# Kernel optimization log

Hardware: AMD Instinct MI355X
Metric: run time of the kernel (lower is better)

The kernel has to match this reference:

```python
import jax, jax.numpy as jnp
import numpy as np

EPS = 1e-6

def rms_norm(x, scale):
    # qwen3_compatible: compute in fp32 (inputs already fp32)
    ms = jnp.mean(x * x, axis=-1, keepdims=True)
    return x * jax.lax.rsqrt(ms + EPS) * scale

def apply_rope(x, cos, sin):
    # x: [b, h, s, hd]; cos/sin: [s, hd]
    hd = x.shape[-1]
    x1, x2 = x[..., : hd // 2], x[..., hd // 2 :]
    rotated = jnp.concatenate([-x2, x1], axis=-1)
    return x * cos[None, None] + rotated * sin[None, None]

def setup_inputs() -> dict:
    key = jax.random.key(0)
    ks = jax.random.split(key, 8)
    b, s, d_in, nh, kv, hd = 2, 2048, 2048, 16, 4, 128
    d_out = nh * hd
    x = jax.random.normal(ks[0], (b, s, d_in), jnp.float32)
    # causal mask: True = masked (future positions)
    mask = jnp.triu(jnp.ones((s, s), bool), k=1)
    # RoPE tables (standard rotary frequencies)
    inv_freq = 1.0 / (10000.0 ** (np.arange(0, hd, 2, dtype=np.float32) / hd))
    angles = np.arange(s, dtype=np.float32)[:, None] * inv_freq[None, :]  # [s, hd/2]
    angles = np.concatenate([angles, angles], axis=1)  # [s, hd]
    cos = jnp.asarray(np.cos(angles))
    sin = jnp.asarray(np.sin(angles))
    sc = 0.02
    Wq = jax.random.normal(ks[1], (d_in, d_out), jnp.float32) * sc
    Wk = jax.random.normal(ks[2], (d_in, kv * hd), jnp.float32) * sc
    Wv = jax.random.normal(ks[3], (d_in, kv * hd), jnp.float32) * sc
    Wo = jax.random.normal(ks[4], (d_out, d_in), jnp.float32) * sc
    q_scale = jnp.ones((hd,), jnp.float32)
    k_scale = jnp.ones((hd,), jnp.float32)
    return {"x": x, "mask": mask, "cos": cos, "sin": sin, "Wq": Wq, "Wk": Wk,
            "Wv": Wv, "Wo": Wo, "q_scale": q_scale, "k_scale": k_scale}

def reference(x, mask, cos, sin, Wq, Wk, Wv, Wo, q_scale, k_scale):
    b, s, d_in = x.shape
    nh, kv, hd = 16, 4, 128
    g = nh // kv  # group_size
    # projections (Linear, no bias); weights stored as [in, out]
    q = (x @ Wq).reshape(b, s, nh, hd).transpose(0, 2, 1, 3)   # [b, nh, s, hd]
    k = (x @ Wk).reshape(b, s, kv, hd).transpose(0, 2, 1, 3)   # [b, kv, s, hd]
    v = (x @ Wv).reshape(b, s, kv, hd).transpose(0, 2, 1, 3)   # [b, kv, s, hd]
    q = rms_norm(q, q_scale)
    k = rms_norm(k, k_scale)
    q = apply_rope(q, cos, sin)
    k = apply_rope(k, cos, sin)
    # group queries: head h uses kv group h // g (repeat_interleave semantics)
    qg = q.reshape(b, kv, g, s, hd)
    scores = jnp.einsum('bkgqh,bkth->bkgqt', qg, k) / jnp.sqrt(jnp.float32(hd))
    scores = jnp.where(mask[None, None, None], -jnp.inf, scores)
    w = jax.nn.softmax(scores, axis=-1)
    ctx = jnp.einsum('bkgqt,bkth->bkgqh', w, v)                # [b, kv, g, s, hd]
    ctx = ctx.reshape(b, nh, s, hd).transpose(0, 2, 1, 3).reshape(b, s, nh * hd)
    return ctx @ Wo
```

## Files before the change

### kernel.cpp

```cpp
#include <hip/hip_runtime.h>
#include <hip/hip_bf16.h>
#include <math.h>

#define B  2
#define S  2048
#define D  2048
#define NH 16
#define KV 4
#define HD 128
#define G  (NH / KV)
#define M_ROWS (B * S)

typedef __hip_bfloat16 bf16;
typedef __attribute__((ext_vector_type(8))) short s16x8;
typedef __attribute__((ext_vector_type(4))) float f32x4;

__device__ __forceinline__ short bf16_bits(float f) {
    bf16 t = __float2bfloat16(f);
    return *reinterpret_cast<short*>(&t);
}

__device__ __forceinline__ void gload16(const void* g, void* l) {
    __builtin_amdgcn_global_load_lds(
        (const __attribute__((address_space(1))) void*)g,
        (__attribute__((address_space(3))) void*)l, 16, 0, 0);
}

__global__ __launch_bounds__(256) void cast_f32_bf16(const float* __restrict__ in,
                                                     bf16* __restrict__ o, int n4) {
    int i = blockIdx.x * 256 + threadIdx.x;
    if (i >= n4) return;
    float4 v = ((const float4*)in)[i];
    ushort4 u;
    u.x = (unsigned short)bf16_bits(v.x);
    u.y = (unsigned short)bf16_bits(v.y);
    u.z = (unsigned short)bf16_bits(v.z);
    u.w = (unsigned short)bf16_bits(v.w);
    ((ushort4*)o)[i] = u;
}

__global__ __launch_bounds__(256) void tcast(const float* __restrict__ W,
                                             bf16* __restrict__ Wt, int K, int N) {
    __shared__ float T[32][33];
    const int n0 = blockIdx.x * 32, k0 = blockIdx.y * 32;
    const int tx = threadIdx.x & 31, ty = threadIdx.x >> 5;
#pragma unroll
    for (int i = 0; i < 4; i++)
        T[ty + i * 8][tx] = W[(size_t)(k0 + ty + i * 8) * N + n0 + tx];
    __syncthreads();
#pragma unroll
    for (int i = 0; i < 4; i++)
        Wt[(size_t)(n0 + ty + i * 8) * K + k0 + tx] = __float2bfloat16(T[tx][ty + i * 8]);
}

template<int MODE>
__global__ __launch_bounds__(256) void gemm_bt(const bf16* __restrict__ A,
                                               const bf16* __restrict__ Bt,
                                               void* __restrict__ out0,
                                               void* __restrict__ out1,
                                               void* __restrict__ out2,
                                               int N, int K) {
    const int m0 = blockIdx.y * 128;
    const int n0 = blockIdx.x * 128;
    const int tid  = threadIdx.x;
    const int wave = tid >> 6;
    const int lane = tid & 63;
    const int mw = (wave >> 1) * 64;
    const int nw = (wave & 1) * 64;

    __shared__ short Al[128 * 32];
    __shared__ short Bl[128 * 32];

    f32x4 acc[4][4] = {};

    const int fr = lane & 15;
    const int fq = (lane >> 4) * 8;

    const int r0  = wave * 32;
    const int srl = lane >> 2;
    const int scl = (lane & 3) * 8;

    for (int k0 = 0; k0 < K; k0 += 32) {
        __syncthreads();
        gload16(A  + (size_t)(m0 + r0 +      srl) * K + k0 + scl, &Al[(r0     ) * 32]);
        gload16(A  + (size_t)(m0 + r0 + 16 + srl) * K + k0 + scl, &Al[(r0 + 16) * 32]);
        gload16(Bt + (size_t)(n0 + r0 +      srl) * K + k0 + scl, &Bl[(r0     ) * 32]);
        gload16(Bt + (size_t)(n0 + r0 + 16 + srl) * K + k0 + scl, &Bl[(r0 + 16) * 32]);
        __syncthreads();

        s16x8 af[4], bfr[4];
#pragma unroll
        for (int i = 0; i < 4; i++) {
            af[i]  = *(const s16x8*)(&Al[(mw + i * 16 + fr) * 32 + fq]);
            bfr[i] = *(const s16x8*)(&Bl[(nw + i * 16 + fr) * 32 + fq]);
        }
#pragma unroll
        for (int i = 0; i < 4; i++)
#pragma unroll
            for (int j = 0; j < 4; j++)
                acc[i][j] = __builtin_amdgcn_mfma_f32_16x16x32_bf16(af[i], bfr[j], acc[i][j], 0, 0, 0);
    }

    const int col_l = lane & 15;
    const int row_l = (lane >> 4) * 4;
#pragma unroll
    for (int i = 0; i < 4; i++)
#pragma unroll
        for (int j = 0; j < 4; j++) {
            int m_base = m0 + mw + i * 16 + row_l;
            int n = n0 + nw + j * 16 + col_l;
            if (MODE == 3 && n >= 2560) {
                int nn = n - 2560;
                int bb = m_base >> 11, si = m_base & (S - 1);
                int hh = nn >> 7, d = nn & (HD - 1);
                ushort4 u;
                u.x = (unsigned short)bf16_bits(acc[i][j][0]);
                u.y = (unsigned short)bf16_bits(acc[i][j][1]);
                u.z = (unsigned short)bf16_bits(acc[i][j][2]);
                u.w = (unsigned short)bf16_bits(acc[i][j][3]);
                *(ushort4*)((bf16*)out2 + (((size_t)(bb * KV + hh)) * HD + d) * S + si) = u;
            } else {
#pragma unroll
                for (int r = 0; r < 4; r++) {
                    int m = m_base + r;
                    if (MODE == 3) {
                        int bb = m >> 11, si = m & (S - 1);
                        if (n < 2048) {
                            int h = n >> 7, d = n & (HD - 1);
                            ((float*)out0)[(((size_t)(bb * NH + h)) * S + si) * HD + d] = acc[i][j][r];
                        } else {
                            int nn = n - 2048;
                            int h = nn >> 7, d = nn & (HD - 1);
                            ((float*)out1)[(((size_t)(bb * KV + h)) * S + si) * HD + d] = acc[i][j][r];
                        }
                    } else {
                        ((float*)out0)[(size_t)m * N + n] = acc[i][j][r];
                    }
                }
            }
        }
}

template<bool SC>
__global__ __launch_bounds__(256) void rms_rope2(const float* __restrict__ in,
                                                 bf16* __restrict__ out,
                                                 const float* __restrict__ scale,
                                                 const float* __restrict__ cosT,
                                                 const float* __restrict__ sinT) {
    const int row  = blockIdx.x * 4 + (threadIdx.x >> 6);
    const int lane = threadIdx.x & 63;
    const int si   = row & (S - 1);
    const float* rp = in + (size_t)row * HD;

    float x1 = rp[lane];
    float x2 = rp[lane + 64];

    float ss = x1 * x1 + x2 * x2;
#pragma unroll
    for (int m = 1; m < 64; m <<= 1) ss += __shfl_xor(ss, m, 64);
    const float rinv = rsqrtf(ss * (1.0f / HD) + 1e-6f);

    const float n1 = x1 * rinv * scale[lane];
    const float n2 = x2 * rinv * scale[lane + 64];

    const float c = cosT[(size_t)si * HD + lane];
    const float s = sinT[(size_t)si * HD + lane];

    float r1 = n1 * c - n2 * s;
    float r2 = n2 * c + n1 * s;
    if (SC) { r1 *= 0.08838834764831845f; r2 *= 0.08838834764831845f; }

    out[(size_t)row * HD + lane]      = __float2bfloat16(r1);
    out[(size_t)row * HD + lane + 64] = __float2bfloat16(r2);
}

__global__ __launch_bounds__(512) void flash_mfma4(const bf16* __restrict__ qb,
                                                   const bf16* __restrict__ kb,
                                                   const bf16* __restrict__ vtb,
                                                   bf16* __restrict__ ctx) {
    const int p    = blockIdx.x;
    const int kvh  = blockIdx.y;
    const int b    = blockIdx.z;
    const int tid  = threadIdx.x;
    const int wave = tid >> 6;
    const int grp  = wave >> 2;
    const int wl   = wave & 3;
    const int lane = tid & 63;
    const int tg   = tid & 255;
    const int quad = lane >> 4;
    const int l16  = lane & 15;
    const int quad8 = quad * 8;
    const int h = kvh * G + wl;

    __shared__ __align__(16) char pool[108544];
    short* KsG = (short*)(pool + grp * 17408);
    short* VsG = (short*)(pool + 34816 + grp * 18432);
    short* PsW = (short*)(pool + 71680 + wave * 4608);
    float* oS  = (float*)pool;
    float* lS  = (float*)(pool + 65536);

    const bf16* qbase = qb  + ((size_t)(b * NH + h))   * S * HD;
    const bf16* kbase = kb  + ((size_t)(b * KV + kvh)) * S * HD;
    const bf16* vbase = vtb + ((size_t)(b * KV + kvh)) * HD * S;

    const int nA   = (p >> 1) + 1;
    const int pB   = 63 - p;
    const int iBeg = grp ? 17 : 0;
    const int iEnd = grp ? 33 : 17;

    int q0 = grp ? 32 * pB : 32 * p;

    s16x8 qf[2][4];
#pragma unroll
    for (int s = 0; s < 2; s++) {
        const bf16* qrow = qbase + (size_t)(q0 + s * 16 + l16) * HD + quad8;
#pragma unroll
        for (int ks = 0; ks < 4; ks++)
            qf[s][ks] = *(const s16x8*)(qrow + ks * 32);
    }

    f32x4 o[2][8] = {};
    float l[2][4] = {};

    uint4 kreg[4], vreg[4];
    {
        const int tf = (iBeg < nA) ? 64 * iBeg : 64 * (iBeg - nA);
#pragma unroll
        for (int it = 0; it < 4; it++) {
            int c = tg + it * 256;
            kreg[it] = *(const uint4*)(kbase + (size_t)(tf + (c >> 4)) * HD + (c & 15) * 8);
            vreg[it] = *(const uint4*)(vbase + (size_t)(c >> 3) * S + tf + (c & 7) * 8);
        }
    }

    for (int ii = 0; ii < 17; ii++) {
        const int i   = iBeg + ii;
        const bool act = (i < iEnd);

        if (act) {
#pragma unroll
            for (int it = 0; it < 4; it++) {
                int c = tg + it * 256;
                *(uint4*)&KsG[(c >> 4) * 136 + (c & 15) * 8] = kreg[it];
                *(uint4*)&VsG[(c >> 3) * 72  + (c & 7)  * 8] = vreg[it];
            }
        }
        __syncthreads();

        const int t0 = (i < nA) ? 64 * i : 64 * (i - nA);

        if (act && i + 1 < iEnd) {
            const int tn = (i + 1 < nA) ? 64 * (i + 1) : 64 * (i + 1 - nA);
#pragma unroll
            for (int it = 0; it < 4; it++) {
                int c = tg + it * 256;
                kreg[it] = *(const uint4*)(kbase + (size_t)(tn + (c >> 4)) * HD + (c & 15) * 8);
                vreg[it] = *(const uint4*)(vbase + (size_t)(c >> 3) * S + tn + (c & 7) * 8);
            }
        }

        if (act) {
            f32x4 sa[2][4] = {};
#pragma unroll
            for (int ks = 0; ks < 4; ks++) {
#pragma unroll
                for (int n = 0; n < 4; n++) {
                    s16x8 kf = *(const s16x8*)&KsG[(n * 16 + l16) * 136 + ks * 32 + quad8];
#pragma unroll
                    for (int s = 0; s < 2; s++)
                        sa[s][n] = __builtin_amdgcn_mfma_f32_16x16x32_bf16(qf[s][ks], kf, sa[s][n], 0, 0, 0);
                }
            }

            const bool msk = (t0 + 63 > q0);
#pragma unroll
            for (int s = 0; s < 2; s++)
#pragma unroll
                for (int r = 0; r < 4; r++) {
                    const int qg = q0 + s * 16 + quad * 4 + r;
#pragma unroll
                    for (int n = 0; n < 4; n++) {
                        float v = sa[s][n][r];
                        if (msk && (t0 + n * 16 + l16 > qg)) v = -INFINITY;
                        float pv = __expf(v - 13.0f);
                        l[s][r] += pv;
                        PsW[(s * 16 + quad * 4 + r) * 72 + n * 16 + l16] = bf16_bits(pv);
                    }
                }

#pragma unroll
            for (int ks = 0; ks < 2; ks++) {
                s16x8 vf[8];
#pragma unroll
                for (int n = 0; n < 8; n++)
                    vf[n] = *(const s16x8*)&VsG[(n * 16 + l16) * 72 + ks * 32 + quad8];
#pragma unroll
                for (int s = 0; s < 2; s++) {
                    s16x8 pf = *(const s16x8*)&PsW[(s * 16 + l16) * 72 + ks * 32 + quad8];
#pragma unroll
                    for (int n = 0; n < 8; n++)
                        o[s][n] = __builtin_amdgcn_mfma_f32_16x16x32_bf16(pf, vf[n], o[s][n], 0, 0, 0);
                }
            }

            if (i == nA - 1) {
#pragma unroll
                for (int s = 0; s < 2; s++)
#pragma unroll
                    for (int r = 0; r < 4; r++) {
                        float ls = l[s][r];
#pragma unroll
                        for (int m = 1; m < 16; m <<= 1) ls += __shfl_xor(ls, m, 64);
                        const float inv = 1.0f / ls;
                        const int qg = q0 + s * 16 + quad * 4 + r;
                        bf16* dst = ctx + (((size_t)(b * S + qg)) * NH + h) * HD;
#pragma unroll
                        for (int n = 0; n < 8; n++)
                            dst[n * 16 + l16] = __float2bfloat16(o[s][n][r] * inv);
                    }
                q0 = 32 * pB;
#pragma unroll
                for (int s = 0; s < 2; s++) {
                    const bf16* qrow = qbase + (size_t)(q0 + s * 16 + l16) * HD + quad8;
#pragma unroll
                    for (int ks = 0; ks < 4; ks++)
                        qf[s][ks] = *(const s16x8*)(qrow + ks * 32);
                }
#pragma unroll
                for (int s = 0; s < 2; s++) {
#pragma unroll
                    for (int n = 0; n < 8; n++) o[s][n] = (f32x4){0.f, 0.f, 0.f, 0.f};
#pragma unroll
                    for (int r = 0; r < 4; r++) l[s][r] = 0.0f;
                }
            }
        }

        __syncthreads();
    }

    if (grp == 1) {
        float* oW = oS + wl * 64 * 64;
        float* lW = lS + wl * 8 * 64;
#pragma unroll
        for (int s = 0; s < 2; s++)
#pragma unroll
            for (int n = 0; n < 8; n++)
#pragma unroll
                for (int r = 0; r < 4; r++)
                    oW[((s * 8 + n) * 4 + r) * 64 + lane] = o[s][n][r];
#pragma unroll
        for (int s = 0; s < 2; s++)
#pragma unroll
            for (int r = 0; r < 4; r++)
                lW[(s * 4 + r) * 64 + lane] = l[s][r];
    }
    __syncthreads();
    if (grp == 0) {
        float* oW = oS + wl * 64 * 64;
        float* lW = lS + wl * 8 * 64;
#pragma unroll
        for (int s = 0; s < 2; s++)
#pragma unroll
            for (int r = 0; r < 4; r++) {
                float ls = l[s][r] + lW[(s * 4 + r) * 64 + lane];
#pragma unroll
                for (int m = 1; m < 16; m <<= 1) ls += __shfl_xor(ls, m, 64);
                const float inv = 1.0f / ls;
                const int qg = q0 + s * 16 + quad * 4 + r;
                bf16* dst = ctx + (((size_t)(b * S + qg)) * NH + h) * HD;
#pragma unroll
                for (int n = 0; n < 8; n++)
                    dst[n * 16 + l16] =
                        __float2bfloat16((o[s][n][r] + oW[((s * 8 + n) * 4 + r) * 64 + lane]) * inv);
            }
    }
}

extern "C" void kernel_launch(void* const* d_in, const int* in_sizes, int n_in,
                              void* d_out, int out_size, void* d_ws, size_t ws_size,
                              hipStream_t stream) {
    const float* x    = (const float*)d_in[0];
    const float* cosT = (const float*)d_in[2];
    const float* sinT = (const float*)d_in[3];
    const float* Wq   = (const float*)d_in[4];
    const float* Wk   = (const float*)d_in[5];
    const float* Wv   = (const float*)d_in[6];
    const float* Wo   = (const float*)d_in[7];
    const float* qsc  = (const float*)d_in[8];
    const float* ksc  = (const float*)d_in[9];
    float* out = (float*)d_out;

    char* w = (char*)d_ws;
    float* q_ws = (float*)(w);
    bf16*  wo_t = (bf16*)(w);
    bf16*  ctx_b= (bf16*)(w + (8u << 20));
    float* k_ws = (float*)(w + (32u << 20));
    bf16*  xb   = (bf16*)(w + (40u << 20));
    bf16*  qb   = (bf16*)(w + (40u << 20));
    bf16*  wq_t = (bf16*)(w + (56u << 20));
    bf16*  kb   = (bf16*)(w + (56u << 20));
    bf16*  wk_t = (bf16*)(w + (64u << 20));
    bf16*  wv_t = (bf16*)(w + (66u << 20));
    bf16*  vtb  = (bf16*)(w + (68u << 20));

    cast_f32_bf16<<<(M_ROWS * D / 4 + 255) / 256, 256, 0, stream>>>(x, xb, M_ROWS * D / 4);
    tcast<<<dim3((NH * HD) / 32, D / 32), 256, 0, stream>>>(Wq, wq_t, D, NH * HD);
    tcast<<<dim3((KV * HD) / 32, D / 32), 256, 0, stream>>>(Wk, wk_t, D, KV * HD);
    tcast<<<dim3((KV * HD) / 32, D / 32), 256, 0, stream>>>(Wv, wv_t, D, KV * HD);

    gemm_bt<3><<<dim3((NH * HD + 2 * KV * HD) / 128, M_ROWS / 128), 256, 0, stream>>>(
        xb, wq_t, q_ws, k_ws, vtb, NH * HD + 2 * KV * HD, D);

    rms_rope2<true ><<<B * NH * S / 4, 256, 0, stream>>>(q_ws, qb, qsc, cosT, sinT);
    rms_rope2<false><<<B * KV * S / 4, 256, 0, stream>>>(k_ws, kb, ksc, cosT, sinT);

    tcast<<<dim3(D / 32, D / 32), 256, 0, stream>>>(Wo, wo_t, D, D);

    flash_mfma4<<<dim3(32, KV, B), 512, 0, stream>>>(qb, kb, vtb, ctx_b);

    gemm_bt<0><<<dim3(D / 128, M_ROWS / 128), 256, 0, stream>>>(ctx_b, wo_t, out, nullptr, nullptr, D, D);
}
```

Measured before the change: 393.8 us.

## Replace paired-tile two-group flash kernel with one 32-row tile per block

```diff
diff --git a/kernel.cpp b/kernel.cpp
--- a/kernel.cpp
+++ b/kernel.cpp
@@ -174,41 +174,31 @@
     out[(size_t)row * HD + lane + 64] = __float2bfloat16(r2);
 }
 
-__global__ __launch_bounds__(512) void flash_mfma4(const bf16* __restrict__ qb,
-                                                   const bf16* __restrict__ kb,
-                                                   const bf16* __restrict__ vtb,
-                                                   bf16* __restrict__ ctx) {
-    const int p    = blockIdx.x;
+__global__ __launch_bounds__(256, 3) void flash_mfma5(const bf16* __restrict__ qb,
+                                                      const bf16* __restrict__ kb,
+                                                      const bf16* __restrict__ vtb,
+                                                      bf16* __restrict__ ctx) {
+    const int t    = 63 - blockIdx.x;
     const int kvh  = blockIdx.y;
     const int b    = blockIdx.z;
     const int tid  = threadIdx.x;
     const int wave = tid >> 6;
-    const int grp  = wave >> 2;
-    const int wl   = wave & 3;
     const int lane = tid & 63;
-    const int tg   = tid & 255;
     const int quad = lane >> 4;
     const int l16  = lane & 15;
     const int quad8 = quad * 8;
-    const int h = kvh * G + wl;
-
-    __shared__ __align__(16) char pool[108544];
-    short* KsG = (short*)(pool + grp * 17408);
-    short* VsG = (short*)(pool + 34816 + grp * 18432);
-    short* PsW = (short*)(pool + 71680 + wave * 4608);
-    float* oS  = (float*)pool;
-    float* lS  = (float*)(pool + 65536);
+    const int h = kvh * G + wave;
+
+    __shared__ short Ks[64][136];
+    __shared__ short Vs[128][72];
+    __shared__ short Ps[4][32][72];
 
     const bf16* qbase = qb  + ((size_t)(b * NH + h))   * S * HD;
     const bf16* kbase = kb  + ((size_t)(b * KV + kvh)) * S * HD;
     const bf16* vbase = vtb + ((size_t)(b * KV + kvh)) * HD * S;
 
-    const int nA   = (p >> 1) + 1;
-    const int pB   = 63 - p;
-    const int iBeg = grp ? 17 : 0;
-    const int iEnd = grp ? 33 : 17;
-
-    int q0 = grp ? 32 * pB : 32 * p;
+    const int nT = (t >> 1) + 1;
+    const int q0 = 32 * t;
 
     s16x8 qf[2][4];
 #pragma unroll
@@ -223,158 +213,94 @@
     float l[2][4] = {};
 
     uint4 kreg[4], vreg[4];
-    {
-        const int tf = (iBeg < nA) ? 64 * iBeg : 64 * (iBeg - nA);
+#pragma unroll
+    for (int it = 0; it < 4; it++) {
+        int c = tid + it * 256;
+        kreg[it] = *(const uint4*)(kbase + (size_t)(c >> 4) * HD + (c & 15) * 8);
+        vreg[it] = *(const uint4*)(vbase + (size_t)(c >> 3) * S + (c & 7) * 8);
+    }
+
+    for (int i = 0; i < nT; i++) {
 #pragma unroll
         for (int it = 0; it < 4; it++) {
-            int c = tg + it * 256;
-            kreg[it] = *(const uint4*)(kbase + (size_t)(tf + (c >> 4)) * HD + (c & 15) * 8);
-            vreg[it] = *(const uint4*)(vbase + (size_t)(c >> 3) * S + tf + (c & 7) * 8);
-        }
-    }
-
-    for (int ii = 0; ii < 17; ii++) {
-        const int i   = iBeg + ii;
-        const bool act = (i < iEnd);
-
-        if (act) {
+            int c = tid + it * 256;
+            *(uint4*)&Ks[c >> 4][(c & 15) * 8] = kreg[it];
+            *(uint4*)&Vs[c >> 3][(c & 7) * 8] = vreg[it];
+        }
+        __syncthreads();
+
+        const int t0 = 64 * i;
+
+        if (i + 1 < nT) {
+            const int tn = 64 * (i + 1);
 #pragma unroll
             for (int it = 0; it < 4; it++) {
-                int c = tg + it * 256;
-                *(uint4*)&KsG[(c >> 4) * 136 + (c & 15) * 8] = kreg[it];
-                *(uint4*)&VsG[(c >> 3) * 72  + (c & 7)  * 8] = vreg[it];
-            }
-        }
-        __syncthreads();
-
-        const int t0 = (i < nA) ? 64 * i : 64 * (i - nA);
-
-        if (act && i + 1 < iEnd) {
-            const int tn = (i + 1 < nA) ? 64 * (i + 1) : 64 * (i + 1 - nA);
-#pragma unroll
-            for (int it = 0; it < 4; it++) {
-                int c = tg + it * 256;
+                int c = tid + it * 256;
                 kreg[it] = *(const uint4*)(kbase + (size_t)(tn + (c >> 4)) * HD + (c & 15) * 8);
                 vreg[it] = *(const uint4*)(vbase + (size_t)(c >> 3) * S + tn + (c & 7) * 8);
             }
         }
 
-        if (act) {
-            f32x4 sa[2][4] = {};
-#pragma unroll
-            for (int ks = 0; ks < 4; ks++) {
+        f32x4 sa[2][4] = {};
+#pragma unroll
+        for (int ks = 0; ks < 4; ks++) {
+#pragma unroll
+            for (int n = 0; n < 4; n++) {
+                s16x8 kf = *(const s16x8*)&Ks[n * 16 + l16][ks * 32 + quad8];
+#pragma unroll
+                for (int s = 0; s < 2; s++)
+                    sa[s][n] = __builtin_amdgcn_mfma_f32_16x16x32_bf16(qf[s][ks], kf, sa[s][n], 0, 0, 0);
+            }
+        }
+
+        const bool msk = (t0 + 63 > q0);
+#pragma unroll
+        for (int s = 0; s < 2; s++)
+#pragma unroll
+            for (int r = 0; r < 4; r++) {
+                const int qg = q0 + s * 16 + quad * 4 + r;
 #pragma unroll
                 for (int n = 0; n < 4; n++) {
-                    s16x8 kf = *(const s16x8*)&KsG[(n * 16 + l16) * 136 + ks * 32 + quad8];
-#pragma unroll
-                    for (int s = 0; s < 2; s++)
-                        sa[s][n] = __builtin_amdgcn_mfma_f32_16x16x32_bf16(qf[s][ks], kf, sa[s][n], 0, 0, 0);
+                    float v = sa[s][n][r];
+                    if (msk && (t0 + n * 16 + l16 > qg)) v = -INFINITY;
+                    float pv = __expf(v - 13.0f);
+                    l[s][r] += pv;
+                    Ps[wave][s * 16 + quad * 4 + r][n * 16 + l16] = bf16_bits(pv);
                 }
             }
 
-            const bool msk = (t0 + 63 > q0);
-#pragma unroll
-            for (int s = 0; s < 2; s++)
-#pragma unroll
-                for (int r = 0; r < 4; r++) {
-                    const int qg = q0 + s * 16 + quad * 4 + r;
-#pragma unroll
-                    for (int n = 0; n < 4; n++) {
-                        float v = sa[s][n][r];
-                        if (msk && (t0 + n * 16 + l16 > qg)) v = -INFINITY;
-                        float pv = __expf(v - 13.0f);
-                        l[s][r] += pv;
-                        PsW[(s * 16 + quad * 4 + r) * 72 + n * 16 + l16] = bf16_bits(pv);
-                    }
-                }
-
-#pragma unroll
-            for (int ks = 0; ks < 2; ks++) {
-                s16x8 vf[8];
+#pragma unroll
+        for (int ks = 0; ks < 2; ks++) {
+            s16x8 vf[8];
+#pragma unroll
+            for (int n = 0; n < 8; n++)
+                vf[n] = *(const s16x8*)&Vs[n * 16 + l16][ks * 32 + quad8];
+#pragma unroll
+            for (int s = 0; s < 2; s++) {
+                s16x8 pf = *(const s16x8*)&Ps[wave][s * 16 + l16][ks * 32 + quad8];
 #pragma unroll
                 for (int n = 0; n < 8; n++)
-                    vf[n] = *(const s16x8*)&VsG[(n * 16 + l16) * 72 + ks * 32 + quad8];
-#pragma unroll
-                for (int s = 0; s < 2; s++) {
-                    s16x8 pf = *(const s16x8*)&PsW[(s * 16 + l16) * 72 + ks * 32 + quad8];
-#pragma unroll
-                    for (int n = 0; n < 8; n++)
-                        o[s][n] = __builtin_amdgcn_mfma_f32_16x16x32_bf16(pf, vf[n], o[s][n], 0, 0, 0);
-                }
-            }
-
-            if (i == nA - 1) {
-#pragma unroll
-                for (int s = 0; s < 2; s++)
-#pragma unroll
-                    for (int r = 0; r < 4; r++) {
-                        float ls = l[s][r];
-#pragma unroll
-                        for (int m = 1; m < 16; m <<= 1) ls += __shfl_xor(ls, m, 64);
-                        const float inv = 1.0f / ls;
-                        const int qg = q0 + s * 16 + quad * 4 + r;
-                        bf16* dst = ctx + (((size_t)(b * S + qg)) * NH + h) * HD;
-#pragma unroll
-                        for (int n = 0; n < 8; n++)
-                            dst[n * 16 + l16] = __float2bfloat16(o[s][n][r] * inv);
-                    }
-                q0 = 32 * pB;
-#pragma unroll
-                for (int s = 0; s < 2; s++) {
-                    const bf16* qrow = qbase + (size_t)(q0 + s * 16 + l16) * HD + quad8;
-#pragma unroll
-                    for (int ks = 0; ks < 4; ks++)
-                        qf[s][ks] = *(const s16x8*)(qrow + ks * 32);
-                }
-#pragma unroll
-                for (int s = 0; s < 2; s++) {
-#pragma unroll
-                    for (int n = 0; n < 8; n++) o[s][n] = (f32x4){0.f, 0.f, 0.f, 0.f};
-#pragma unroll
-                    for (int r = 0; r < 4; r++) l[s][r] = 0.0f;
-                }
+                    o[s][n] = __builtin_amdgcn_mfma_f32_16x16x32_bf16(pf, vf[n], o[s][n], 0, 0, 0);
             }
         }
 
         __syncthreads();
     }
 
-    if (grp == 1) {
-        float* oW = oS + wl * 64 * 64;
-        float* lW = lS + wl * 8 * 64;
-#pragma unroll
-        for (int s = 0; s < 2; s++)
+#pragma unroll
+    for (int s = 0; s < 2; s++)
+#pragma unroll
+        for (int r = 0; r < 4; r++) {
+            float ls = l[s][r];
+#pragma unroll
+            for (int m = 1; m < 16; m <<= 1) ls += __shfl_xor(ls, m, 64);
+            const float inv = 1.0f / ls;
+            const int qg = q0 + s * 16 + quad * 4 + r;
+            bf16* dst = ctx + (((size_t)(b * S + qg)) * NH + h) * HD;
 #pragma unroll
             for (int n = 0; n < 8; n++)
-#pragma unroll
-                for (int r = 0; r < 4; r++)
-                    oW[((s * 8 + n) * 4 + r) * 64 + lane] = o[s][n][r];
-#pragma unroll
-        for (int s = 0; s < 2; s++)
-#pragma unroll
-            for (int r = 0; r < 4; r++)
-                lW[(s * 4 + r) * 64 + lane] = l[s][r];
-    }
-    __syncthreads();
-    if (grp == 0) {
-        float* oW = oS + wl * 64 * 64;
-        float* lW = lS + wl * 8 * 64;
-#pragma unroll
-        for (int s = 0; s < 2; s++)
-#pragma unroll
-            for (int r = 0; r < 4; r++) {
-                float ls = l[s][r] + lW[(s * 4 + r) * 64 + lane];
-#pragma unroll
-                for (int m = 1; m < 16; m <<= 1) ls += __shfl_xor(ls, m, 64);
-                const float inv = 1.0f / ls;
-                const int qg = q0 + s * 16 + quad * 4 + r;
-                bf16* dst = ctx + (((size_t)(b * S + qg)) * NH + h) * HD;
-#pragma unroll
-                for (int n = 0; n < 8; n++)
-                    dst[n * 16 + l16] =
-                        __float2bfloat16((o[s][n][r] + oW[((s * 8 + n) * 4 + r) * 64 + lane]) * inv);
-            }
-    }
+                dst[n * 16 + l16] = __float2bfloat16(o[s][n][r] * inv);
+        }
 }
 
 extern "C" void kernel_launch(void* const* d_in, const int* in_sizes, int n_in,
@@ -417,7 +343,7 @@
 
     tcast<<<dim3(D / 32, D / 32), 256, 0, stream>>>(Wo, wo_t, D, D);
 
-    flash_mfma4<<<dim3(32, KV, B), 512, 0, stream>>>(qb, kb, vtb, ctx_b);
+    flash_mfma5<<<dim3(64, KV, B), 256, 0, stream>>>(qb, kb, vtb, ctx_b);
 
     gemm_bt<0><<<dim3(D / 128, M_ROWS / 128), 256, 0, stream>>>(ctx_b, wo_t, out, nullptr, nullptr, D, D);
 }
```

New measurement: 530.7 us. 1.35x slower.
